# Kernel tuning notes

Hardware: AMD Instinct MI355X
Metric: run time of the kernel (lower is better)

The kernel has to match this reference:

```python
import jax, jax.numpy as jnp
import numpy as np

N_NODES = 100000
N_EDGES = 3200000
HIDDEN = 128
N_CLASSES = 10
N_GRAPHS = 128
EPS = 1e-5


def setup_inputs() -> dict:
    key = jax.random.key(0)
    ks = jax.random.split(key, 16)
    x = jax.random.normal(ks[0], (N_NODES, 1), dtype=jnp.float32)
    edge_index = jax.random.randint(ks[1], (2, N_EDGES), 0, N_NODES, dtype=jnp.int64)
    batch = jnp.sort(jax.random.randint(ks[2], (N_NODES,), 0, N_GRAPHS, dtype=jnp.int64))
    def lin(k, fi, fo):
        s = 1.0 / np.sqrt(fi)
        return jax.random.uniform(k, (fi, fo), jnp.float32, -s, s)
    return {
        "x": x, "edge_index": edge_index, "batch": batch,
        "Wc1": lin(ks[3], 1, HIDDEN), "bc1": jnp.zeros((HIDDEN,), jnp.float32),
        "Wl1": lin(ks[4], 1, HIDDEN), "bl1": jnp.zeros((HIDDEN,), jnp.float32),
        "g1": jnp.ones((HIDDEN,), jnp.float32), "be1": jnp.zeros((HIDDEN,), jnp.float32),
        "Wc2": lin(ks[5], HIDDEN, HIDDEN), "bc2": jnp.zeros((HIDDEN,), jnp.float32),
        "Wl2": lin(ks[6], HIDDEN, HIDDEN), "bl2": jnp.zeros((HIDDEN,), jnp.float32),
        "g2": jnp.ones((HIDDEN,), jnp.float32), "be2": jnp.zeros((HIDDEN,), jnp.float32),
        "W3": lin(ks[7], HIDDEN, N_CLASSES), "b3": jnp.zeros((N_CLASSES,), jnp.float32),
    }


def _gcn_conv(x, W, b, src, dst, n):
    # PyG GCNConv: add self-loops, symmetric normalization, then scatter-add.
    h = x @ W                                    # [N, F]
    loops = jnp.arange(n, dtype=src.dtype)
    s = jnp.concatenate([src, loops])
    d = jnp.concatenate([dst, loops])
    deg = jax.ops.segment_sum(jnp.ones_like(d, dtype=h.dtype), d, num_segments=n)
    dinv = jnp.where(deg > 0, jax.lax.rsqrt(deg), 0.0)
    norm = dinv[s] * dinv[d]                     # [E+N]
    msg = h[s] * norm[:, None]                   # gather + scale
    out = jax.ops.segment_sum(msg, d, num_segments=n)
    return out + b


def _batch_norm(x, gamma, beta):
    mu = jnp.mean(x, axis=0)
    var = jnp.mean(jnp.square(x - mu), axis=0)
    return (x - mu) * jax.lax.rsqrt(var + EPS) * gamma + beta


def reference(x, edge_index, batch, Wc1, bc1, Wl1, bl1, g1, be1,
              Wc2, bc2, Wl2, bl2, g2, be2, W3, b3):
    src, dst = edge_index[0], edge_index[1]
    n = x.shape[0]
    h = _gcn_conv(x, Wc1, bc1, src, dst, n) + (x @ Wl1 + bl1)
    h = jax.nn.relu(h)
    h = _batch_norm(h, g1, be1)
    h = _gcn_conv(h, Wc2, bc2, src, dst, n) + (h @ Wl2 + bl2)
    h = _batch_norm(h, g2, be2)
    # global_mean_pool over graph ids
    sums = jax.ops.segment_sum(h, batch, num_segments=N_GRAPHS)
    cnts = jax.ops.segment_sum(jnp.ones((n,), h.dtype), batch, num_segments=N_GRAPHS)
    pooled = sums / jnp.maximum(cnts, 1.0)[:, None]
    return pooled @ W3 + b3
```

## Files before the change

kernel.cpp:

```cpp
#include <hip/hip_runtime.h>
#include <hip/hip_bf16.h>

__device__ __forceinline__ float bf2f(unsigned short u) {
    union { unsigned int i; float f; } c; c.i = ((unsigned int)u) << 16; return c.f;
}
__device__ __forceinline__ unsigned short f2bf(float f) {
    union { unsigned int i; float f; } c; c.f = f;
    unsigned int i = c.i;
    unsigned int r = (i + 0x7FFFu + ((i >> 16) & 1u)) >> 16;
    return (unsigned short)r;
}
__device__ __forceinline__ float u2f_hi(unsigned int u) {
    union { unsigned int i; float f; } c; c.i = u & 0xFFFF0000u; return c.f;
}
__device__ __forceinline__ float u2f_lo(unsigned int u) {
    union { unsigned int i; float f; } c; c.i = u << 16; return c.f;
}
__device__ __forceinline__ int ldi(const void* p, long long i, int is64) {
    return is64 ? (int)((const long long*)p)[i] : ((const int*)p)[i];
}

typedef __attribute__((ext_vector_type(8))) short short8;
typedef __attribute__((ext_vector_type(4))) float floatx4;

#define HID 128
#define EPS 1e-5f
#define NBK 256
#define CH 4096

#define OF_WC1 0
#define OF_BC1 128
#define OF_WL1 256
#define OF_BL1 384
#define OF_G1  512
#define OF_BE1 640
#define OF_WC2 768
#define OF_BC2 17152
#define OF_WL2 17280
#define OF_BL2 33664
#define OF_G2  33792
#define OF_BE2 33920
#define OF_W3  34048
#define OF_B3  35328
#define N_CANON 35338

__global__ void k_zero(int* __restrict__ p, long long n,
                       const unsigned int* __restrict__ g1w,
                       const unsigned int* __restrict__ eiw,
                       int* __restrict__ flags) {
    long long i = (long long)blockIdx.x * blockDim.x + threadIdx.x;
    if (i < n) p[i] = 0;
    if (blockIdx.x == 0 && threadIdx.x == 0) {
        flags[0] = (g1w[0] == 0x3F800000u) ? 1 : 0;
        flags[1] = (eiw[1] == 0u && eiw[3] == 0u && eiw[5] == 0u) ? 1 : 0;
    }
}

struct ConvArgs { const void* s[14]; float* d[14]; int n[14]; };
__global__ void k_wconv(ConvArgs a, const int* __restrict__ flags) {
    int seg = blockIdx.y;
    int i = blockIdx.x * 256 + threadIdx.x;
    if (i >= a.n[seg]) return;
    float v = flags[0] ? ((const float*)a.s[seg])[i]
                       : bf2f(((const unsigned short*)a.s[seg])[i]);
    a.d[seg][i] = v;
}

__global__ void k_wT(const float* __restrict__ C, unsigned short* __restrict__ W2T) {
    int i = blockIdx.x * 256 + threadIdx.x;
    if (i >= HID * 256) return;
    int f = i >> 8, k = i & 255;
    float w = (k < HID) ? C[OF_WC2 + k * HID + f] : C[OF_WL2 + (k - HID) * HID + f];
    W2T[f * 256 + k] = f2bf(w);
}


__global__ void __launch_bounds__(256) k_bhist(const void* __restrict__ ei, int E, int N,
                                               const int* __restrict__ flags,
                                               int* __restrict__ bcnt) {
    __shared__ int h[NBK];
    int t = threadIdx.x;
    h[t] = 0;
    __syncthreads();
    int is64 = flags[1];
    long long base = (long long)blockIdx.x * CH;
    for (int k = 0; k < CH / 256; k++) {
        long long i = base + k * 256 + t;
        if (i < E) {
            int d = ldi(ei, (long long)E + i, is64);
            if ((unsigned)d < (unsigned)N) atomicAdd(&h[d >> 9], 1);
        }
    }
    __syncthreads();
    if (h[t]) atomicAdd(&bcnt[t], h[t]);
}

__global__ void k_bscan(const int* __restrict__ bcnt, int* __restrict__ boff,
                        int* __restrict__ bcur) {
    __shared__ int sd[NBK];
    int t = threadIdx.x;
    int v = bcnt[t];
    sd[t] = v;
    __syncthreads();
    for (int off = 1; off < NBK; off <<= 1) {
        int add = (t >= off) ? sd[t - off] : 0;
        __syncthreads();
        sd[t] += add;
        __syncthreads();
    }
    int ex = sd[t] - v;
    boff[t] = ex;
    bcur[t] = ex;
}

__global__ void __launch_bounds__(256) k_bpart(const void* __restrict__ ei, int E, int N,
                                               const int* __restrict__ flags,
                                               int* __restrict__ bcur, uint2* __restrict__ pairs) {
    __shared__ uint2 buf[CH];
    __shared__ int h[NBK], sc[NBK], offs[NBK], cur[NBK], gpos[NBK];
    int t = threadIdx.x;
    h[t] = 0;
    __syncthreads();
    int is64 = flags[1];
    long long base = (long long)blockIdx.x * CH;
    int ss[CH / 256], dd[CH / 256];
    bool ok[CH / 256];
#pragma unroll
    for (int k = 0; k < CH / 256; k++) {
        long long i = base + k * 256 + t;
        ok[k] = false; ss[k] = 0; dd[k] = 0;
        if (i < E) {
            int s = ldi(ei, i, is64);
            int d = ldi(ei, (long long)E + i, is64);
            ss[k] = s; dd[k] = d;
            if ((unsigned)s < (unsigned)N && (unsigned)d < (unsigned)N) {
                ok[k] = true;
                atomicAdd(&h[d >> 9], 1);
            }
        }
    }
    __syncthreads();
    int hv = h[t];
    sc[t] = hv;
    __syncthreads();
    for (int off = 1; off < NBK; off <<= 1) {
        int add = (t >= off) ? sc[t - off] : 0;
        __syncthreads();
        sc[t] += add;
        __syncthreads();
    }
    offs[t] = sc[t] - hv;
    cur[t] = sc[t] - hv;
    __syncthreads();
#pragma unroll
    for (int k = 0; k < CH / 256; k++) {
        if (ok[k]) {
            int b = dd[k] >> 9;
            int p = atomicAdd(&cur[b], 1);
            buf[p] = make_uint2((unsigned)ss[k], (unsigned)dd[k]);
        }
    }
    if (hv) gpos[t] = atomicAdd(&bcur[t], hv);
    else gpos[t] = 0;
    __syncthreads();
    int vc = offs[NBK - 1] + h[NBK - 1];
    for (int i = t; i < vc; i += 256) {
        uint2 e = buf[i];
        int lo = (int)(e.y >> 9);
        pairs[(size_t)gpos[lo] + (i - offs[lo])] = e;
    }
}

__global__ void __launch_bounds__(256) k_bcsr(const uint2* __restrict__ pairs,
                                              const int* __restrict__ boff,
                                              const int* __restrict__ bcnt,
                                              int N, int E,
                                              int* __restrict__ deg, int* __restrict__ rowptr,
                                              int* __restrict__ col) {
    __shared__ int cnt[512], lofs[512], lcur[512], part[256];
    int b = blockIdx.x, t = threadIdx.x;
    for (int j = t; j < 512; j += 256) { cnt[j] = 0; lcur[j] = 0; }
    __syncthreads();
    int s0 = boff[b], n = bcnt[b];
    for (int i = t; i < n; i += 256) {
        uint2 p = pairs[(size_t)s0 + i];
        atomicAdd(&cnt[p.y & 511], 1);
    }
    __syncthreads();
    int a0 = cnt[2 * t], a1 = cnt[2 * t + 1];
    part[t] = a0 + a1;
    __syncthreads();
    for (int off = 1; off < 256; off <<= 1) {
        int add = (t >= off) ? part[t - off] : 0;
        __syncthreads();
        part[t] += add;
        __syncthreads();
    }
    int ex = part[t] - (a0 + a1);
    lofs[2 * t] = ex;
    lofs[2 * t + 1] = ex + a0;
    __syncthreads();
    int vb = b << 9;
    for (int j = t; j < 512; j += 256) {
        int v = vb + j;
        if (v < N) { deg[v] = cnt[j]; rowptr[v] = s0 + lofs[j]; }
    }
    for (int i = t; i < n; i += 256) {
        uint2 p = pairs[(size_t)s0 + i];
        int dl = p.y & 511;
        int sl = atomicAdd(&lcur[dl], 1);
        int idx = s0 + lofs[dl] + sl;
        if ((unsigned)idx < (unsigned)E) col[idx] = (int)p.x;
    }
}

__global__ void k_prep(const void* __restrict__ x, const int* __restrict__ deg, int N,
                       const int* __restrict__ flags, float* __restrict__ dinv,
                       float* __restrict__ xf, float* __restrict__ xd1, float* __restrict__ rd) {
    int i = blockIdx.x * blockDim.x + threadIdx.x;
    if (i < N) {
        float dp1 = (float)(max(deg[i], 0) + 1);
        float dv = rsqrtf(dp1);
        float xv = flags[0] ? ((const float*)x)[i] : bf2f(((const unsigned short*)x)[i]);
        dinv[i] = dv;
        xf[i] = xv;
        xd1[i] = xv * dv;
        rd[i] = sqrtf(dp1);
    }
}

__global__ void __launch_bounds__(256) k_bps(const uint2* __restrict__ pairs,
                                             const int* __restrict__ boff,
                                             const int* __restrict__ bcnt,
                                             const float* __restrict__ xd1,
                                             const float* __restrict__ xf,
                                             const float* __restrict__ dinv,
                                             int N, float4* __restrict__ node) {
    __shared__ float psL[512];
    int b = blockIdx.x, t = threadIdx.x;
    for (int j = t; j < 512; j += 256) psL[j] = 0.f;
    __syncthreads();
    int s0 = boff[b], n = bcnt[b];
    for (int i = t; i < n; i += 256) {
        uint2 p = pairs[(size_t)s0 + i];
        atomicAdd(&psL[p.y & 511], xd1[p.x]);
    }
    __syncthreads();
    int vb = b << 9;
    for (int j = t; j < 512; j += 256) {
        int v = vb + j;
        if (v < N) {
            float dv = dinv[v], xv = xf[v];
            node[v] = make_float4(dv * (psL[j] + xv * dv), xv, dv, 0.f);
        }
    }
}

#define ROWS1 128
__global__ void k_stats1(const float4* __restrict__ node, const float* __restrict__ C,
                         int N, float* __restrict__ S1, float* __restrict__ S2) {
    int f = threadIdx.x;
    float wc = C[OF_WC1 + f], wl = C[OF_WL1 + f];
    float b = C[OF_BC1 + f] + C[OF_BL1 + f];
    int v0 = blockIdx.x * ROWS1;
    float s1 = 0.f, s2 = 0.f;
    for (int r = 0; r < ROWS1; r++) {
        int v = v0 + r;
        if (v >= N) break;
        float4 nd = node[v];
        float h = fmaxf(nd.x * wc + nd.y * wl + b, 0.f);
        s1 += h; s2 += h * h;
    }
    atomicAdd(&S1[f], s1);
    atomicAdd(&S2[f], s2);
}

__global__ void k_bn1(const float* __restrict__ S1, const float* __restrict__ S2,
                      const float* __restrict__ C, int N, float* __restrict__ ab) {
    int f = threadIdx.x;
    float mu = S1[f] / (float)N;
    float var = S2[f] / (float)N - mu * mu;
    float a = C[OF_G1 + f] * rsqrtf(fmaxf(var, 0.f) + EPS);
    ab[f] = a;
    ab[HID + f] = C[OF_BE1 + f] - mu * a;
}

__global__ void k_zmat(const float4* __restrict__ node, const float* __restrict__ C,
                       const float* __restrict__ ab, int N, unsigned int* __restrict__ zd) {
    int i = blockIdx.x * blockDim.x + threadIdx.x;
    if (i >= N * 64) return;
    int v = i >> 6, c = i & 63;
    float4 nd = node[v];
    int f0 = c * 2, f1 = f0 + 1;
    float z0 = ab[f0] * fmaxf(nd.x * C[OF_WC1 + f0] + nd.y * C[OF_WL1 + f0]
                              + C[OF_BC1 + f0] + C[OF_BL1 + f0], 0.f) + ab[HID + f0];
    float z1 = ab[f1] * fmaxf(nd.x * C[OF_WC1 + f1] + nd.y * C[OF_WL1 + f1]
                              + C[OF_BC1 + f1] + C[OF_BL1 + f1], 0.f) + ab[HID + f1];
    float dv = nd.z;
    zd[i] = (unsigned)f2bf(dv * z0) | ((unsigned)f2bf(dv * z1) << 16);
}

#define RGF 32
__global__ void __launch_bounds__(256) k_fgg(
        const float4* __restrict__ node, const int* __restrict__ col,
        const int* __restrict__ rowptr, const int* __restrict__ deg,
        const float* __restrict__ ab,
        const unsigned short* __restrict__ W2T, const float* __restrict__ C,
        const void* __restrict__ batch, const int* __restrict__ flags,
        int N, int E,
        float* __restrict__ S1b, float* __restrict__ S2b, float* __restrict__ G) {
    __shared__ unsigned short azL[RGF * 264];
    int t = threadIdx.x;
    int wave = t >> 6, lane = t & 63;
    int vbase = blockIdx.x * RGF;
    int is64 = flags[1];
    if (vbase >= N) return;

    int f0 = 2 * lane, f1 = f0 + 1;
    float wc10 = C[OF_WC1 + f0], wl10 = C[OF_WL1 + f0];
    float wc11 = C[OF_WC1 + f1], wl11 = C[OF_WL1 + f1];
    float b10 = C[OF_BC1 + f0] + C[OF_BL1 + f0];
    float b11 = C[OF_BC1 + f1] + C[OF_BL1 + f1];
    float a10 = ab[f0], be10 = ab[HID + f0];
    float a11 = ab[f1], be11 = ab[HID + f1];

    auto zacc = [&](float4 n, float& a0, float& a1) {
        float z0 = fmaf(a10, fmaxf(fmaf(n.x, wc10, fmaf(n.y, wl10, b10)), 0.f), be10);
        float z1 = fmaf(a11, fmaxf(fmaf(n.x, wc11, fmaf(n.y, wl11, b11)), 0.f), be11);
        a0 = fmaf(n.z, z0, a0);
        a1 = fmaf(n.z, z1, a1);
    };

    for (int r = 0; r < 8; r++) {
        int row = wave * 8 + r;
        int v = vbase + row;
        unsigned aggp = 0, zp = 0;
        if (v < N) {
            float4 nv = node[v];
            float z0v = fmaf(a10, fmaxf(fmaf(nv.x, wc10, fmaf(nv.y, wl10, b10)), 0.f), be10);
            float z1v = fmaf(a11, fmaxf(fmaf(nv.x, wc11, fmaf(nv.y, wl11, b11)), 0.f), be11);
            float a0 = nv.z * z0v, a1 = nv.z * z1v;
            int base = max(rowptr[v], 0);
            int dn = max(0, min(deg[v], E - base));
            base = __builtin_amdgcn_readfirstlane(base);
            dn = __builtin_amdgcn_readfirstlane(dn);
            int j = 0;
            int head = min(dn, (4 - (base & 3)) & 3);
            for (; j < head; j++) {
                int s = col[base + j];
                if ((unsigned)s >= (unsigned)N) s = 0;
                zacc(node[s], a0, a1);
            }
            for (; j + 8 <= dn; j += 8) {
                int4 ca = *(const int4*)&col[base + j];
                int4 cb = *(const int4*)&col[base + j + 4];
                int s0 = ca.x, s1 = ca.y, s2 = ca.z, s3 = ca.w;
                int s4 = cb.x, s5 = cb.y, s6 = cb.z, s7 = cb.w;
                if ((unsigned)s0 >= (unsigned)N) s0 = 0;
                if ((unsigned)s1 >= (unsigned)N) s1 = 0;
                if ((unsigned)s2 >= (unsigned)N) s2 = 0;
                if ((unsigned)s3 >= (unsigned)N) s3 = 0;
                if ((unsigned)s4 >= (unsigned)N) s4 = 0;
                if ((unsigned)s5 >= (unsigned)N) s5 = 0;
                if ((unsigned)s6 >= (unsigned)N) s6 = 0;
                if ((unsigned)s7 >= (unsigned)N) s7 = 0;
                float4 n0 = node[s0], n1 = node[s1], n2 = node[s2], n3 = node[s3];
                float4 n4 = node[s4], n5 = node[s5], n6 = node[s6], n7 = node[s7];
                zacc(n0, a0, a1); zacc(n1, a0, a1); zacc(n2, a0, a1); zacc(n3, a0, a1);
                zacc(n4, a0, a1); zacc(n5, a0, a1); zacc(n6, a0, a1); zacc(n7, a0, a1);
            }
            for (; j + 4 <= dn; j += 4) {
                int4 cc = *(const int4*)&col[base + j];
                int s0 = cc.x, s1 = cc.y, s2 = cc.z, s3 = cc.w;
                if ((unsigned)s0 >= (unsigned)N) s0 = 0;
                if ((unsigned)s1 >= (unsigned)N) s1 = 0;
                if ((unsigned)s2 >= (unsigned)N) s2 = 0;
                if ((unsigned)s3 >= (unsigned)N) s3 = 0;
                float4 n0 = node[s0], n1 = node[s1], n2 = node[s2], n3 = node[s3];
                zacc(n0, a0, a1); zacc(n1, a0, a1); zacc(n2, a0, a1); zacc(n3, a0, a1);
            }
            for (; j < dn; j++) {
                int s = col[base + j];
                if ((unsigned)s >= (unsigned)N) s = 0;
                zacc(node[s], a0, a1);
            }
            aggp = (unsigned)f2bf(nv.z * a0) | ((unsigned)f2bf(nv.z * a1) << 16);
            zp   = (unsigned)f2bf(z0v) | ((unsigned)f2bf(z1v) << 16);
        }
        *(unsigned*)&azL[row * 264 + 2 * lane] = aggp;
        *(unsigned*)&azL[row * 264 + 128 + 2 * lane] = zp;
    }
    __syncthreads();

    int quad = lane >> 4, m = lane & 15;
    int half = wave >> 1, tg = wave & 1;
    int rbase = half * 16;
    short8 afr[8];
#pragma unroll
    for (int kb = 0; kb < 8; kb++)
        afr[kb] = *(const short8*)&azL[(rbase + m) * 264 + kb * 32 + quad * 8];

    int vlast = min(vbase + RGF - 1, N - 1);
    bool uni = (ldi(batch, vbase, is64) == ldi(batch, vlast, is64));

    float ps1[4], ps2[4], pgs[4];
#pragma unroll
    for (int ftl = 0; ftl < 4; ftl++) {
        int ft = tg * 4 + ftl;
        floatx4 acc = {0.f, 0.f, 0.f, 0.f};
        const unsigned short* brow = &W2T[(ft * 16 + m) * 256];
#pragma unroll
        for (int kb = 0; kb < 8; kb++) {
            short8 bfr = *(const short8*)&brow[kb * 32 + quad * 8];
            acc = __builtin_amdgcn_mfma_f32_16x16x32_bf16(afr[kb], bfr, acc, 0, 0, 0);
        }
        int cgl = ft * 16 + m;
        float bbv = C[OF_BC2 + cgl] + C[OF_BL2 + cgl];
        float s1 = 0.f, s2 = 0.f, gs = 0.f;
#pragma unroll
        for (int reg = 0; reg < 4; reg++) {
            int v = vbase + rbase + quad * 4 + reg;
            if (v < N) {
                float h = acc[reg] + bbv;
                s1 += h; s2 += h * h;
                if (uni) gs += h;
                else {
                    int g = ldi(batch, v, is64);
                    if ((unsigned)g < 128u) atomicAdd(&G[g * HID + cgl], h);
                }
            }
        }
        ps1[ftl] = s1; ps2[ftl] = s2; pgs[ftl] = gs;
    }

    __syncthreads();
    float* red = (float*)azL;
    int contrib = half * 4 + quad;
#pragma unroll
    for (int ftl = 0; ftl < 4; ftl++) {
        int cgl = (tg * 4 + ftl) * 16 + m;
        red[contrib * 128 + cgl]        = ps1[ftl];
        red[1024 + contrib * 128 + cgl] = ps2[ftl];
        red[2048 + contrib * 128 + cgl] = pgs[ftl];
    }
    __syncthreads();
    if (t < HID) {
        float a1 = 0.f, a2 = 0.f, ag = 0.f;
#pragma unroll
        for (int w = 0; w < 8; w++) {
            a1 += red[w * 128 + t];
            a2 += red[1024 + w * 128 + t];
            ag += red[2048 + w * 128 + t];
        }
        atomicAdd(&S1b[t], a1);
        atomicAdd(&S2b[t], a2);
        if (uni) {
            int g = ldi(batch, vbase, is64);
            if ((unsigned)g < 128u) atomicAdd(&G[g * HID + t], ag);
        }
    }
}

__global__ void __launch_bounds__(256) k_gather2(
        const unsigned int* __restrict__ zd, const int* __restrict__ col,
        const int* __restrict__ rowptr, const int* __restrict__ deg,
        const float* __restrict__ dinv, int N, int E, int c0r, int c1r,
        unsigned int* __restrict__ agg) {
    int gt = blockIdx.x * 256 + threadIdx.x;
    int w = gt >> 6, lane = gt & 63;
    int v = c0r + w;
    if (v >= c1r || v >= N) return;
    int base = max(rowptr[v], 0);
    int dn = max(0, min(deg[v], E - base));
    unsigned int us = zd[(size_t)v * 64 + lane];
    float a0 = u2f_lo(us), a1 = u2f_hi(us);
    for (int j = 0; j < dn; j++) {
        int s = col[base + j];
        if ((unsigned)s >= (unsigned)N) s = 0;
        unsigned int u = zd[(size_t)s * 64 + lane];
        a0 += u2f_lo(u); a1 += u2f_hi(u);
    }
    float dv = dinv[v];
    agg[(size_t)(v - c0r) * 64 + lane] = (unsigned)f2bf(dv * a0) | ((unsigned)f2bf(dv * a1) << 16);
}

#define RG 32
__global__ void __launch_bounds__(128) k_gemm3(
        const unsigned int* __restrict__ zd, const unsigned int* __restrict__ agg,
        const float* __restrict__ rd, const unsigned short* __restrict__ W2T,
        const float* __restrict__ C,
        const void* __restrict__ batch, const int* __restrict__ flags,
        int N, int c0r, int c1r,
        float* __restrict__ S1b, float* __restrict__ S2b, float* __restrict__ G) {
    __shared__ char smem[32 * 264 * 2];
    unsigned short* azL = (unsigned short*)smem;
    int t = threadIdx.x;
    int vbase = c0r + blockIdx.x * RG;
    int vend = min(c1r, N);
    int is64 = flags[1];
    if (vbase >= vend) return;

    for (int it = 0; it < 16; it++) {
        int idx = it * 128 + t;
        int r = idx >> 6, c = idx & 63;
        int v = vbase + r;
        unsigned ua = 0, uz = 0; float rv = 0.f;
        if (v < vend) {
            ua = agg[(size_t)(v - c0r) * 64 + c];
            uz = zd[(size_t)v * 64 + c];
            rv = rd[v];
        }
        *(unsigned*)&azL[r * 264 + 2 * c] = ua;
        float z0 = u2f_lo(uz) * rv, z1 = u2f_hi(uz) * rv;
        *(unsigned*)&azL[r * 264 + 128 + 2 * c] =
            (unsigned)f2bf(z0) | ((unsigned)f2bf(z1) << 16);
    }
    __syncthreads();

    int wave = t >> 6, lane = t & 63, quad = lane >> 4, m = lane & 15;

    short8 afr[8];
#pragma unroll
    for (int kb = 0; kb < 8; kb++)
        afr[kb] = *(const short8*)&azL[(wave * 16 + m) * 264 + kb * 32 + quad * 8];

    int vlast = min(vbase + RG - 1, vend - 1);
    bool uni = (ldi(batch, vbase, is64) == ldi(batch, vlast, is64));

    float ps1[8], ps2[8], pgs[8];
#pragma unroll
    for (int ft = 0; ft < 8; ft++) {
        floatx4 acc = {0.f, 0.f, 0.f, 0.f};
        const unsigned short* brow = &W2T[(ft * 16 + m) * 256];
#pragma unroll
        for (int kb = 0; kb < 8; kb++) {
            short8 bfr = *(const short8*)&brow[kb * 32 + quad * 8];
            acc = __builtin_amdgcn_mfma_f32_16x16x32_bf16(afr[kb], bfr, acc, 0, 0, 0);
        }
        int cgl = ft * 16 + m;
        float bbv = C[OF_BC2 + cgl] + C[OF_BL2 + cgl];
        float s1 = 0.f, s2 = 0.f, gs = 0.f;
#pragma unroll
        for (int reg = 0; reg < 4; reg++) {
            int v = vbase + wave * 16 + quad * 4 + reg;
            if (v < vend) {
                float h = acc[reg] + bbv;
                s1 += h; s2 += h * h;
                if (uni) gs += h;
                else {
                    int g = ldi(batch, v, is64);
                    if ((unsigned)g < 128u) atomicAdd(&G[g * HID + cgl], h);
                }
            }
        }
        ps1[ft] = s1; ps2[ft] = s2; pgs[ft] = gs;
    }

    __syncthreads();
    float* red = (float*)smem;
    int wq = wave * 4 + quad;
#pragma unroll
    for (int ft = 0; ft < 8; ft++) {
        int cgl = ft * 16 + m;
        red[wq * 128 + cgl]        = ps1[ft];
        red[1024 + wq * 128 + cgl] = ps2[ft];
        red[2048 + wq * 128 + cgl] = pgs[ft];
    }
    __syncthreads();
    if (t < HID) {
        float a1 = 0.f, a2 = 0.f, ag = 0.f;
#pragma unroll
        for (int w = 0; w < 8; w++) {
            a1 += red[w * 128 + t];
            a2 += red[1024 + w * 128 + t];
            ag += red[2048 + w * 128 + t];
        }
        atomicAdd(&S1b[t], a1);
        atomicAdd(&S2b[t], a2);
        if (uni) {
            int g = ldi(batch, vbase, is64);
            if ((unsigned)g < 128u) atomicAdd(&G[g * HID + t], ag);
        }
    }
}

__global__ void k_deg(const void* __restrict__ ei, int E, int N, const int* __restrict__ flags,
                      int* __restrict__ deg, int* __restrict__ slot) {
    int i = blockIdx.x * blockDim.x + threadIdx.x;
    if (i < E) {
        int d = ldi(ei, (long long)E + i, flags[1]);
        int sl = ((unsigned)d < (unsigned)N) ? atomicAdd(&deg[d], 1) : 0;
        slot[i] = sl;
    }
}
__global__ void k_scanA(const int* __restrict__ deg, int N, int* __restrict__ rowptr,
                        int* __restrict__ bsum) {
    __shared__ int sd[256];
    int t = threadIdx.x;
    int i = blockIdx.x * 256 + t;
    int my = (i < N) ? deg[i] : 0;
    sd[t] = my;
    __syncthreads();
    for (int off = 1; off < 256; off <<= 1) {
        int add = (t >= off) ? sd[t - off] : 0;
        __syncthreads();
        sd[t] += add;
        __syncthreads();
    }
    if (i < N) rowptr[i] = sd[t] - my;
    if (t == 255) bsum[blockIdx.x] = sd[255];
}
__global__ void k_scanB(int* __restrict__ bsum, int NB) {
    __shared__ int sd[512];
    int t = threadIdx.x;
    if (NB <= 512) {
        int v = (t < NB) ? bsum[t] : 0;
        sd[t] = v;
        __syncthreads();
        for (int off = 1; off < 512; off <<= 1) {
            int add = (t >= off) ? sd[t - off] : 0;
            __syncthreads();
            sd[t] += add;
            __syncthreads();
        }
        if (t < NB) bsum[t] = sd[t] - v;
    } else if (t == 0) {
        int run = 0;
        for (int b = 0; b < NB; b++) { int v = bsum[b]; bsum[b] = run; run += v; }
    }
}
__global__ void k_scanC(int* __restrict__ rowptr, const int* __restrict__ bsum, int N) {
    int i = blockIdx.x * blockDim.x + threadIdx.x;
    if (i < N) rowptr[i] += bsum[i >> 8];
}
__global__ void k_fill(const void* __restrict__ ei, int E, int N, const int* __restrict__ flags,
                       const int* __restrict__ rowptr, const int* __restrict__ slot,
                       int* __restrict__ col, const float* __restrict__ xd1,
                       float* __restrict__ ps) {
    int i = blockIdx.x * blockDim.x + threadIdx.x;
    if (i < E) {
        int is64 = flags[1];
        int s = ldi(ei, i, is64);
        int d = ldi(ei, (long long)E + i, is64);
        if ((unsigned)s < (unsigned)N && (unsigned)d < (unsigned)N) {
            int idx = rowptr[d] + slot[i];
            if ((unsigned)idx < (unsigned)E) col[idx] = s;
            atomicAdd(&ps[d], xd1[s]);
        }
    }
}
__global__ void k_node3(const float* __restrict__ xf, const float* __restrict__ ps,
                        const float* __restrict__ dinv, int N, float4* __restrict__ node) {
    int i = blockIdx.x * blockDim.x + threadIdx.x;
    if (i < N) {
        float dv = dinv[i];
        float xv = xf[i];
        node[i] = make_float4(dv * (ps[i] + xv * dv), xv, dv, 0.f);
    }
}

__global__ void k_out(const float* __restrict__ G,
                      const float* __restrict__ S1b, const float* __restrict__ S2b,
                      const float* __restrict__ C, const int* __restrict__ flags,
                      const void* __restrict__ batch,
                      int N, void* __restrict__ out) {
    __shared__ float pb[HID];
    int f = threadIdx.x;
    int g = blockIdx.x;
    int is64 = flags[1];
    auto lb = [&](int tv) {
        int lo = 0, hi = N;
        while (lo < hi) { int m = (lo + hi) >> 1; if (ldi(batch, m, is64) < tv) lo = m + 1; else hi = m; }
        return lo;
    };
    float cgc = fmaxf((float)(lb(g + 1) - lb(g)), 1.f);
    float mu = S1b[f] / (float)N;
    float var = S2b[f] / (float)N - mu * mu;
    float a = C[OF_G2 + f] * rsqrtf(fmaxf(var, 0.f) + EPS);
    float be = C[OF_BE2 + f] - mu * a;
    pb[f] = a * (G[g * HID + f] / cgc) + be;
    __syncthreads();
    if (f < 10) {
        float s = C[OF_B3 + f];
        for (int k = 0; k < HID; k++) s += pb[k] * C[OF_W3 + k * 10 + f];
        if (flags[0]) ((float*)out)[g * 10 + f] = s;
        else ((unsigned short*)out)[g * 10 + f] = f2bf(s);
    }
}

extern "C" void kernel_launch(void* const* d_in, const int* in_sizes, int n_in,
                              void* d_out, int out_size, void* d_ws, size_t ws_size,
                              hipStream_t stream) {
    const void* x   = d_in[0];
    const void* ei  = d_in[1];
    const void* bat = d_in[2];
    const void* w_src[14] = { d_in[3], d_in[4], d_in[5], d_in[6], d_in[7], d_in[8],
                              d_in[9], d_in[10], d_in[11], d_in[12], d_in[13], d_in[14],
                              d_in[15], d_in[16] };
    const int w_cnt[14] = { 128,128,128,128,128,128, 16384,128,16384,128,128,128, 1280,10 };

    const int N = in_sizes[0];
    const int E = in_sizes[1] / 2;
    const int NB = (N + 255) / 256;

    char* ws = (char*)d_ws;
    size_t off = 0;
    auto alloc = [&](size_t bytes) -> void* {
        void* p = ws + off;
        off = (off + bytes + 255) & ~(size_t)255;
        return p;
    };
    float* S1a  = (float*)alloc(HID * 4);
    float* S2a  = (float*)alloc(HID * 4);
    float* S1b  = (float*)alloc(HID * 4);
    float* S2b  = (float*)alloc(HID * 4);
    float* G    = (float*)alloc(128 * HID * 4);
    int*   bsum = (int*)  alloc(2048);
    int*   bcnt = (int*)  alloc(NBK * 4);
    size_t zbytes = off;
    int*    flags  = (int*)   alloc(256);
    float*  canon  = (float*) alloc(N_CANON * 4);
    unsigned short* W2T = (unsigned short*)alloc(HID * 256 * 2);
    float*  xf     = (float*) alloc((size_t)N * 4);
    float*  dinv   = (float*) alloc((size_t)N * 4);
    float*  xd1    = (float*) alloc((size_t)N * 4);
    float*  rd     = (float*) alloc((size_t)N * 4);
    float4* node   = (float4*)alloc((size_t)N * 16);
    int*    deg    = (int*)   alloc((size_t)N * 4);
    float*  ps     = (float*) alloc((size_t)N * 4);
    int*    rowptr = (int*)   alloc((size_t)N * 4);
    int*    boff   = (int*)   alloc(NBK * 4);
    int*    bcur   = (int*)   alloc(NBK * 4);
    float*  ab     = (float*) alloc(2 * HID * 4);
    size_t ebytes = ((size_t)E * 8 > (size_t)N * 256) ? (size_t)E * 8 : (size_t)N * 256;
    char*   edgebuf = (char*) alloc(ebytes);
    int*    col    = (int*)   alloc((size_t)E * 4);
    size_t fastNeed = off;
    unsigned int* zd = (unsigned int*)alloc((size_t)N * 256);
    unsigned int* aggSep = (unsigned int*)alloc((size_t)N * 256);
    size_t fbNeed = off;

    uint2* pairs = (uint2*)edgebuf;
    int* colFB = (int*)edgebuf;
    int* slotFB = (int*)(edgebuf + (size_t)E * 4);
    (void)n_in; (void)out_size;

    bool fastB = (ws_size >= fastNeed) && (N <= 131072);

    ConvArgs ca;
    int w_off[14] = { OF_WC1, OF_BC1, OF_WL1, OF_BL1, OF_G1, OF_BE1,
                      OF_WC2, OF_BC2, OF_WL2, OF_BL2, OF_G2, OF_BE2, OF_W3, OF_B3 };
    for (int i = 0; i < 14; i++) { ca.s[i] = w_src[i]; ca.d[i] = canon + w_off[i]; ca.n[i] = w_cnt[i]; }

    const int tb = 256;
    long long zn = (long long)(zbytes / 4);
    k_zero  <<<(int)((zn + tb - 1) / tb), tb, 0, stream>>>((int*)d_ws, zn,
                                                           (const unsigned int*)d_in[7],
                                                           (const unsigned int*)ei, flags);
    k_wconv <<<dim3(64, 14), 256, 0, stream>>>(ca, flags);
    k_wT    <<<(HID * 256 + tb - 1) / tb, tb, 0, stream>>>(canon, W2T);

    if (fastB) {
        const int NCH = (E + CH - 1) / CH;
        const int nbk = (N + 511) >> 9;
        k_bhist<<<NCH, 256, 0, stream>>>(ei, E, N, flags, bcnt);
        k_bscan<<<1, NBK, 0, stream>>>(bcnt, boff, bcur);
        k_bpart<<<NCH, 256, 0, stream>>>(ei, E, N, flags, bcur, pairs);
        k_bcsr <<<nbk, 256, 0, stream>>>(pairs, boff, bcnt, N, E, deg, rowptr, col);
        k_prep <<<(N + tb - 1) / tb, tb, 0, stream>>>(x, deg, N, flags, dinv, xf, xd1, rd);
        k_bps  <<<nbk, 256, 0, stream>>>(pairs, boff, bcnt, xd1, xf, dinv, N, node);
        k_stats1<<<(N + ROWS1 - 1) / ROWS1, HID, 0, stream>>>(node, canon, N, S1a, S2a);
        k_bn1  <<<1, HID, 0, stream>>>(S1a, S2a, canon, N, ab);
        k_fgg  <<<(N + RGF - 1) / RGF, 256, 0, stream>>>(node, col, rowptr, deg, ab, W2T,
                                                         canon, bat, flags, N, E, S1b, S2b, G);
    } else {
        bool haveAgg = (ws_size >= fbNeed);
        unsigned int* agg = haveAgg ? aggSep : (unsigned int*)edgebuf;
        k_zero<<<(2 * N + tb - 1) / tb, tb, 0, stream>>>(deg, 2 * N,
                                                         (const unsigned int*)d_in[7],
                                                         (const unsigned int*)ei, flags);
        k_deg  <<<(E + tb - 1) / tb, tb, 0, stream>>>(ei, E, N, flags, deg, slotFB);
        k_prep <<<(N + tb - 1) / tb, tb, 0, stream>>>(x, deg, N, flags, dinv, xf, xd1, rd);
        k_scanA<<<NB, 256, 0, stream>>>(deg, N, rowptr, bsum);
        k_scanB<<<1, 512, 0, stream>>>(bsum, NB);
        k_scanC<<<NB, 256, 0, stream>>>(rowptr, bsum, N);
        k_fill <<<(E + tb - 1) / tb, tb, 0, stream>>>(ei, E, N, flags, rowptr, slotFB, colFB, xd1, ps);
        k_node3<<<(N + tb - 1) / tb, tb, 0, stream>>>(xf, ps, dinv, N, node);
        k_stats1<<<(N + ROWS1 - 1) / ROWS1, HID, 0, stream>>>(node, canon, N, S1a, S2a);
        k_bn1  <<<1, HID, 0, stream>>>(S1a, S2a, canon, N, ab);
        k_zmat <<<(N * 64 + tb - 1) / tb, tb, 0, stream>>>(node, canon, ab, N, zd);
        k_gather2<<<((size_t)N * 64 + tb - 1) / tb, tb, 0, stream>>>(zd, colFB, rowptr, deg, dinv,
                                                                     N, E, 0, N, agg);
        k_gemm3<<<(N + RG - 1) / RG, 128, 0, stream>>>(zd, agg, rd, W2T, canon, bat, flags,
                                                       N, 0, N, S1b, S2b, G);
    }
    k_out<<<128, HID, 0, stream>>>(G, S1b, S2b, canon, flags, bat, N, d_out);
}
```

Baseline: 451.6 us.

## Fuse prep, stats and BN1 kernels into CSR build and partial-sum kernels

Folds the weight transpose into the weight conversion kernel and computes dinv, xf and xd1 inside the CSR build kernel. The first-layer batch-norm statistics are now accumulated inside the partial-sum kernel from shared memory, and the BN1 coefficients are derived inside the fused gather kernel. This drops four kernel launches on the fast path and avoids re-reading the node array for statistics. In exchange, every fgg block recomputes the BN coefficients redundantly, and per-block atomics on the stats now run at 512-node granularity.

```diff
diff --git a/kernel.cpp b/kernel.cpp
--- a/kernel.cpp
+++ b/kernel.cpp
@@ -57,21 +57,16 @@
 }
 
 struct ConvArgs { const void* s[14]; float* d[14]; int n[14]; };
-__global__ void k_wconv(ConvArgs a, const int* __restrict__ flags) {
+__global__ void k_wconv(ConvArgs a, const int* __restrict__ flags,
+                        unsigned short* __restrict__ W2T) {
     int seg = blockIdx.y;
     int i = blockIdx.x * 256 + threadIdx.x;
     if (i >= a.n[seg]) return;
     float v = flags[0] ? ((const float*)a.s[seg])[i]
                        : bf2f(((const unsigned short*)a.s[seg])[i]);
     a.d[seg][i] = v;
-}
-
-__global__ void k_wT(const float* __restrict__ C, unsigned short* __restrict__ W2T) {
-    int i = blockIdx.x * 256 + threadIdx.x;
-    if (i >= HID * 256) return;
-    int f = i >> 8, k = i & 255;
-    float w = (k < HID) ? C[OF_WC2 + k * HID + f] : C[OF_WL2 + (k - HID) * HID + f];
-    W2T[f * 256 + k] = f2bf(w);
+    if (seg == 6) W2T[(i & 127) * 256 + (i >> 7)] = f2bf(v);
+    else if (seg == 8) W2T[(i & 127) * 256 + 128 + (i >> 7)] = f2bf(v);
 }
 
 
@@ -174,9 +169,13 @@
 __global__ void __launch_bounds__(256) k_bcsr(const uint2* __restrict__ pairs,
                                               const int* __restrict__ boff,
                                               const int* __restrict__ bcnt,
+                                              const void* __restrict__ x,
+                                              const int* __restrict__ flags,
                                               int N, int E,
                                               int* __restrict__ deg, int* __restrict__ rowptr,
-                                              int* __restrict__ col) {
+                                              int* __restrict__ col,
+                                              float* __restrict__ dinv, float* __restrict__ xf,
+                                              float* __restrict__ xd1) {
     __shared__ int cnt[512], lofs[512], lcur[512], part[256];
     int b = blockIdx.x, t = threadIdx.x;
     for (int j = t; j < 512; j += 256) { cnt[j] = 0; lcur[j] = 0; }
@@ -201,9 +200,19 @@
     lofs[2 * t + 1] = ex + a0;
     __syncthreads();
     int vb = b << 9;
+    int isf32 = flags[0];
     for (int j = t; j < 512; j += 256) {
         int v = vb + j;
-        if (v < N) { deg[v] = cnt[j]; rowptr[v] = s0 + lofs[j]; }
+        if (v < N) {
+            int dg = cnt[j];
+            deg[v] = dg;
+            rowptr[v] = s0 + lofs[j];
+            float dv = rsqrtf((float)(dg + 1));
+            float xv = isf32 ? ((const float*)x)[v] : bf2f(((const unsigned short*)x)[v]);
+            dinv[v] = dv;
+            xf[v] = xv;
+            xd1[v] = xv * dv;
+        }
     }
     for (int i = t; i < n; i += 256) {
         uint2 p = pairs[(size_t)s0 + i];
@@ -214,29 +223,16 @@
     }
 }
 
-__global__ void k_prep(const void* __restrict__ x, const int* __restrict__ deg, int N,
-                       const int* __restrict__ flags, float* __restrict__ dinv,
-                       float* __restrict__ xf, float* __restrict__ xd1, float* __restrict__ rd) {
-    int i = blockIdx.x * blockDim.x + threadIdx.x;
-    if (i < N) {
-        float dp1 = (float)(max(deg[i], 0) + 1);
-        float dv = rsqrtf(dp1);
-        float xv = flags[0] ? ((const float*)x)[i] : bf2f(((const unsigned short*)x)[i]);
-        dinv[i] = dv;
-        xf[i] = xv;
-        xd1[i] = xv * dv;
-        rd[i] = sqrtf(dp1);
-    }
-}
-
 __global__ void __launch_bounds__(256) k_bps(const uint2* __restrict__ pairs,
                                              const int* __restrict__ boff,
                                              const int* __restrict__ bcnt,
                                              const float* __restrict__ xd1,
                                              const float* __restrict__ xf,
                                              const float* __restrict__ dinv,
-                                             int N, float4* __restrict__ node) {
-    __shared__ float psL[512];
+                                             const float* __restrict__ C,
+                                             int N, float4* __restrict__ node,
+                                             float* __restrict__ S1a, float* __restrict__ S2a) {
+    __shared__ float psL[512], xL[512];
     int b = blockIdx.x, t = threadIdx.x;
     for (int j = t; j < 512; j += 256) psL[j] = 0.f;
     __syncthreads();
@@ -251,60 +247,32 @@
         int v = vb + j;
         if (v < N) {
             float dv = dinv[v], xv = xf[v];
-            node[v] = make_float4(dv * (psL[j] + xv * dv), xv, dv, 0.f);
-        }
-    }
-}
-
-#define ROWS1 128
-__global__ void k_stats1(const float4* __restrict__ node, const float* __restrict__ C,
-                         int N, float* __restrict__ S1, float* __restrict__ S2) {
-    int f = threadIdx.x;
+            float p = dv * (psL[j] + xv * dv);
+            node[v] = make_float4(p, xv, dv, 0.f);
+            psL[j] = p;
+            xL[j] = xv;
+        } else { psL[j] = 0.f; xL[j] = 0.f; }
+    }
+    __syncthreads();
+    int f = t & 127, hh = t >> 7;
     float wc = C[OF_WC1 + f], wl = C[OF_WL1 + f];
-    float b = C[OF_BC1 + f] + C[OF_BL1 + f];
-    int v0 = blockIdx.x * ROWS1;
+    float bb = C[OF_BC1 + f] + C[OF_BL1 + f];
+    int jend = min(512, N - vb);
+    int j0 = hh * 256, j1 = min(j0 + 256, jend);
     float s1 = 0.f, s2 = 0.f;
-    for (int r = 0; r < ROWS1; r++) {
-        int v = v0 + r;
-        if (v >= N) break;
-        float4 nd = node[v];
-        float h = fmaxf(nd.x * wc + nd.y * wl + b, 0.f);
+    for (int j = j0; j < j1; j++) {
+        float h = fmaxf(fmaf(psL[j], wc, fmaf(xL[j], wl, bb)), 0.f);
         s1 += h; s2 += h * h;
     }
-    atomicAdd(&S1[f], s1);
-    atomicAdd(&S2[f], s2);
-}
-
-__global__ void k_bn1(const float* __restrict__ S1, const float* __restrict__ S2,
-                      const float* __restrict__ C, int N, float* __restrict__ ab) {
-    int f = threadIdx.x;
-    float mu = S1[f] / (float)N;
-    float var = S2[f] / (float)N - mu * mu;
-    float a = C[OF_G1 + f] * rsqrtf(fmaxf(var, 0.f) + EPS);
-    ab[f] = a;
-    ab[HID + f] = C[OF_BE1 + f] - mu * a;
-}
-
-__global__ void k_zmat(const float4* __restrict__ node, const float* __restrict__ C,
-                       const float* __restrict__ ab, int N, unsigned int* __restrict__ zd) {
-    int i = blockIdx.x * blockDim.x + threadIdx.x;
-    if (i >= N * 64) return;
-    int v = i >> 6, c = i & 63;
-    float4 nd = node[v];
-    int f0 = c * 2, f1 = f0 + 1;
-    float z0 = ab[f0] * fmaxf(nd.x * C[OF_WC1 + f0] + nd.y * C[OF_WL1 + f0]
-                              + C[OF_BC1 + f0] + C[OF_BL1 + f0], 0.f) + ab[HID + f0];
-    float z1 = ab[f1] * fmaxf(nd.x * C[OF_WC1 + f1] + nd.y * C[OF_WL1 + f1]
-                              + C[OF_BC1 + f1] + C[OF_BL1 + f1], 0.f) + ab[HID + f1];
-    float dv = nd.z;
-    zd[i] = (unsigned)f2bf(dv * z0) | ((unsigned)f2bf(dv * z1) << 16);
+    atomicAdd(&S1a[f], s1);
+    atomicAdd(&S2a[f], s2);
 }
 
 #define RGF 32
 __global__ void __launch_bounds__(256) k_fgg(
         const float4* __restrict__ node, const int* __restrict__ col,
         const int* __restrict__ rowptr, const int* __restrict__ deg,
-        const float* __restrict__ ab,
+        const float* __restrict__ S1a, const float* __restrict__ S2a,
         const unsigned short* __restrict__ W2T, const float* __restrict__ C,
         const void* __restrict__ batch, const int* __restrict__ flags,
         int N, int E,
@@ -321,8 +289,14 @@
     float wc11 = C[OF_WC1 + f1], wl11 = C[OF_WL1 + f1];
     float b10 = C[OF_BC1 + f0] + C[OF_BL1 + f0];
     float b11 = C[OF_BC1 + f1] + C[OF_BL1 + f1];
-    float a10 = ab[f0], be10 = ab[HID + f0];
-    float a11 = ab[f1], be11 = ab[HID + f1];
+    float mu0 = S1a[f0] / (float)N;
+    float var0 = S2a[f0] / (float)N - mu0 * mu0;
+    float a10 = C[OF_G1 + f0] * rsqrtf(fmaxf(var0, 0.f) + EPS);
+    float be10 = C[OF_BE1 + f0] - mu0 * a10;
+    float mu1 = S1a[f1] / (float)N;
+    float var1 = S2a[f1] / (float)N - mu1 * mu1;
+    float a11 = C[OF_G1 + f1] * rsqrtf(fmaxf(var1, 0.f) + EPS);
+    float be11 = C[OF_BE1 + f1] - mu1 * a11;
 
     auto zacc = [&](float4 n, float& a0, float& a1) {
         float z0 = fmaf(a10, fmaxf(fmaf(n.x, wc10, fmaf(n.y, wl10, b10)), 0.f), be10);
@@ -461,6 +435,65 @@
     }
 }
 
+__global__ void k_prep(const void* __restrict__ x, const int* __restrict__ deg, int N,
+                       const int* __restrict__ flags, float* __restrict__ dinv,
+                       float* __restrict__ xf, float* __restrict__ xd1, float* __restrict__ rd) {
+    int i = blockIdx.x * blockDim.x + threadIdx.x;
+    if (i < N) {
+        float dp1 = (float)(max(deg[i], 0) + 1);
+        float dv = rsqrtf(dp1);
+        float xv = flags[0] ? ((const float*)x)[i] : bf2f(((const unsigned short*)x)[i]);
+        dinv[i] = dv;
+        xf[i] = xv;
+        xd1[i] = xv * dv;
+        rd[i] = sqrtf(dp1);
+    }
+}
+
+#define ROWS1 128
+__global__ void k_stats1(const float4* __restrict__ node, const float* __restrict__ C,
+                         int N, float* __restrict__ S1, float* __restrict__ S2) {
+    int f = threadIdx.x;
+    float wc = C[OF_WC1 + f], wl = C[OF_WL1 + f];
+    float b = C[OF_BC1 + f] + C[OF_BL1 + f];
+    int v0 = blockIdx.x * ROWS1;
+    float s1 = 0.f, s2 = 0.f;
+    for (int r = 0; r < ROWS1; r++) {
+        int v = v0 + r;
+        if (v >= N) break;
+        float4 nd = node[v];
+        float h = fmaxf(nd.x * wc + nd.y * wl + b, 0.f);
+        s1 += h; s2 += h * h;
+    }
+    atomicAdd(&S1[f], s1);
+    atomicAdd(&S2[f], s2);
+}
+
+__global__ void k_bn1(const float* __restrict__ S1, const float* __restrict__ S2,
+                      const float* __restrict__ C, int N, float* __restrict__ ab) {
+    int f = threadIdx.x;
+    float mu = S1[f] / (float)N;
+    float var = S2[f] / (float)N - mu * mu;
+    float a = C[OF_G1 + f] * rsqrtf(fmaxf(var, 0.f) + EPS);
+    ab[f] = a;
+    ab[HID + f] = C[OF_BE1 + f] - mu * a;
+}
+
+__global__ void k_zmat(const float4* __restrict__ node, const float* __restrict__ C,
+                       const float* __restrict__ ab, int N, unsigned int* __restrict__ zd) {
+    int i = blockIdx.x * blockDim.x + threadIdx.x;
+    if (i >= N * 64) return;
+    int v = i >> 6, c = i & 63;
+    float4 nd = node[v];
+    int f0 = c * 2, f1 = f0 + 1;
+    float z0 = ab[f0] * fmaxf(nd.x * C[OF_WC1 + f0] + nd.y * C[OF_WL1 + f0]
+                              + C[OF_BC1 + f0] + C[OF_BL1 + f0], 0.f) + ab[HID + f0];
+    float z1 = ab[f1] * fmaxf(nd.x * C[OF_WC1 + f1] + nd.y * C[OF_WL1 + f1]
+                              + C[OF_BC1 + f1] + C[OF_BL1 + f1], 0.f) + ab[HID + f1];
+    float dv = nd.z;
+    zd[i] = (unsigned)f2bf(dv * z0) | ((unsigned)f2bf(dv * z1) << 16);
+}
+
 __global__ void __launch_bounds__(256) k_gather2(
         const unsigned int* __restrict__ zd, const int* __restrict__ col,
         const int* __restrict__ rowptr, const int* __restrict__ deg,
@@ -757,8 +790,7 @@
     k_zero  <<<(int)((zn + tb - 1) / tb), tb, 0, stream>>>((int*)d_ws, zn,
                                                            (const unsigned int*)d_in[7],
                                                            (const unsigned int*)ei, flags);
-    k_wconv <<<dim3(64, 14), 256, 0, stream>>>(ca, flags);
-    k_wT    <<<(HID * 256 + tb - 1) / tb, tb, 0, stream>>>(canon, W2T);
+    k_wconv <<<dim3(64, 14), 256, 0, stream>>>(ca, flags, W2T);
 
     if (fastB) {
         const int NCH = (E + CH - 1) / CH;
@@ -766,12 +798,11 @@
         k_bhist<<<NCH, 256, 0, stream>>>(ei, E, N, flags, bcnt);
         k_bscan<<<1, NBK, 0, stream>>>(bcnt, boff, bcur);
         k_bpart<<<NCH, 256, 0, stream>>>(ei, E, N, flags, bcur, pairs);
-        k_bcsr <<<nbk, 256, 0, stream>>>(pairs, boff, bcnt, N, E, deg, rowptr, col);
-        k_prep <<<(N + tb - 1) / tb, tb, 0, stream>>>(x, deg, N, flags, dinv, xf, xd1, rd);
-        k_bps  <<<nbk, 256, 0, stream>>>(pairs, boff, bcnt, xd1, xf, dinv, N, node);
-        k_stats1<<<(N + ROWS1 - 1) / ROWS1, HID, 0, stream>>>(node, canon, N, S1a, S2a);
-        k_bn1  <<<1, HID, 0, stream>>>(S1a, S2a, canon, N, ab);
-        k_fgg  <<<(N + RGF - 1) / RGF, 256, 0, stream>>>(node, col, rowptr, deg, ab, W2T,
+        k_bcsr <<<nbk, 256, 0, stream>>>(pairs, boff, bcnt, x, flags, N, E,
+                                         deg, rowptr, col, dinv, xf, xd1);
+        k_bps  <<<nbk, 256, 0, stream>>>(pairs, boff, bcnt, xd1, xf, dinv, canon,
+                                         N, node, S1a, S2a);
+        k_fgg  <<<(N + RGF - 1) / RGF, 256, 0, stream>>>(node, col, rowptr, deg, S1a, S2a, W2T,
                                                          canon, bat, flags, N, E, S1b, S2b, G);
     } else {
         bool haveAgg = (ws_size >= fbNeed);
```

Result: faster. 429.5 us (-4.9%).
